# Performance work log

Measured on AMD Instinct MI355X. Metric: run time of the kernel, lower is better.

Reference implementation:

```python
import jax, jax.numpy as jnp
import numpy as np
from jax import lax

IN_CH = 512
OUT_CH = 512
HEAD_DIM = 8
NUM_HEADS = IN_CH // HEAD_DIM  # 64
INNER = NUM_HEADS * HEAD_DIM   # 512
KSIZE = 5
EPS = 1e-15
BN_EPS = 1e-5
DN = ('NCHW', 'OIHW', 'NCHW')


def setup_inputs() -> dict:
    key = jax.random.key(0)
    ks = jax.random.split(key, 10)
    s = 0.02
    return {
        'hidden_states': jax.random.normal(ks[0], (4, IN_CH, 64, 64), jnp.float32),
        'wq': jax.random.normal(ks[1], (INNER, IN_CH), jnp.float32) * s,
        'wk': jax.random.normal(ks[2], (INNER, IN_CH), jnp.float32) * s,
        'wv': jax.random.normal(ks[3], (INNER, IN_CH), jnp.float32) * s,
        # depthwise conv: groups = 3*INNER, 1 in-channel per group
        'dw_kernel': jax.random.normal(ks[4], (3 * INNER, 1, KSIZE, KSIZE), jnp.float32) * s,
        # grouped 1x1 conv: groups = 3*NUM_HEADS -> 3*INNER/(3*NUM_HEADS)=HEAD_DIM in-ch/group
        'pw_kernel': jax.random.normal(ks[5], (3 * INNER, HEAD_DIM, 1, 1), jnp.float32) * s,
        # proj_out 1x1: in = INNER*(1+len(kernel_sizes)) = 2*INNER
        'proj_kernel': jax.random.normal(ks[6], (OUT_CH, 2 * INNER, 1, 1), jnp.float32) * s,
        'bn_gamma': jnp.ones((OUT_CH,), jnp.float32),
        'bn_beta': jnp.zeros((OUT_CH,), jnp.float32),
        'bn_mean': jnp.zeros((OUT_CH,), jnp.float32),
        'bn_var': jnp.ones((OUT_CH,), jnp.float32),
    }


def _forward(hidden_states, wq, wk, wv, dw_kernel, pw_kernel, proj_kernel,
             bn_gamma, bn_beta, bn_mean, bn_var):
    x = hidden_states  # [B,C,H,W]
    B, _, H, W = x.shape
    h = jnp.moveaxis(x, 1, -1)  # [B,H,W,C]
    q = h @ wq.T
    k = h @ wk.T
    v = h @ wv.T
    qkv = jnp.moveaxis(jnp.concatenate([q, k, v], axis=-1), -1, 1)  # [B,3*INNER,H,W]

    # multi-scale aggregation: depthwise 5x5 then grouped 1x1
    dw = lax.conv_general_dilated(qkv, dw_kernel, (1, 1), 'SAME',
                                  feature_group_count=3 * INNER, dimension_numbers=DN)
    pw = lax.conv_general_dilated(dw, pw_kernel, (1, 1), 'VALID',
                                  feature_group_count=3 * NUM_HEADS, dimension_numbers=DN)
    qkv_all = jnp.concatenate([qkv, pw], axis=1)  # [B, 2*3*INNER, H, W]

    # relu linear attention (fp32)
    N = H * W
    d = HEAD_DIM
    f = qkv_all.astype(jnp.float32).reshape(B, -1, 3 * d, N)  # [B, nh_total, 3d, N]
    query = jax.nn.relu(f[:, :, :d])
    key_ = jax.nn.relu(f[:, :, d:2 * d])
    value = f[:, :, 2 * d:]
    value_pad = jnp.concatenate([value, jnp.ones_like(value[:, :, :1])], axis=2)  # [B,nh,d+1,N]
    scores = jnp.einsum('bhdn,bhen->bhde', value_pad, key_)   # [B,nh,d+1,d]
    out = jnp.einsum('bhde,bhen->bhdn', scores, query)         # [B,nh,d+1,N]
    out = out[:, :, :-1] / (out[:, :, -1:] + EPS)
    out = out.reshape(B, -1, H, W).astype(qkv_all.dtype)        # [B, 2*INNER, H, W]

    # proj_out 1x1 conv + BatchNorm2d (eval mode, running stats)
    y = lax.conv_general_dilated(out, proj_kernel, (1, 1), 'VALID', dimension_numbers=DN)
    inv = bn_gamma / jnp.sqrt(bn_var + BN_EPS)
    y = y * inv[None, :, None, None] + (bn_beta - bn_mean * inv)[None, :, None, None]
    return y + x


def reference(hidden_states, wq, wk, wv, dw_kernel, pw_kernel, proj_kernel,
              bn_gamma, bn_beta, bn_mean, bn_var):
    return _forward(hidden_states, wq, wk, wv, dw_kernel, pw_kernel, proj_kernel,
                    bn_gamma, bn_beta, bn_mean, bn_var)
```

## Files before the change

### kernel.cpp

```cpp
#include <hip/hip_runtime.h>
#include <hip/hip_bf16.h>

typedef __hip_bfloat16 bf16;
typedef __attribute__((ext_vector_type(8))) short bf16x8;
typedef __attribute__((ext_vector_type(4))) float f32x4;
typedef __attribute__((ext_vector_type(2))) float f32x2;

#define BATCH 4
#define CIN   512
#define HW    64
#define NPIX  4096
#define CALL  3072
#define NHEAD 128
#define EPS_LITE 1e-15f
#define BN_EPS   1e-5f
#define LDK   40


__device__ __forceinline__ short f2bf(float f) {
    __hip_bfloat16 h = __float2bfloat16(f);
    short s; __builtin_memcpy(&s, &h, 2); return s;
}
__device__ __forceinline__ float bfl(unsigned u) {
    unsigned v = u << 16; float f; __builtin_memcpy(&f, &v, 4); return f;
}
__device__ __forceinline__ float bfh(unsigned u) {
    unsigned v = u & 0xffff0000u; float f; __builtin_memcpy(&f, &v, 4); return f;
}
__device__ __forceinline__ unsigned packbf(float a, float b) {
    return (unsigned)(unsigned short)f2bf(a) | ((unsigned)(unsigned short)f2bf(b) << 16);
}

template<bool XF32, int KD, bool PROJ>
__global__ __launch_bounds__(256) void k_gemm(
        const void* __restrict__ Xv,
        const float* __restrict__ w0, const float* __restrict__ w1,
        const float* __restrict__ w2,
        bf16* __restrict__ Obf,
        const float* __restrict__ gm, const float* __restrict__ bt,
        const float* __restrict__ mu, const float* __restrict__ va,
        const float* __restrict__ resid, float* __restrict__ Of)
{
    constexpr int NT = KD / 32;
    __shared__ short Ald[2][64 * LDK];
    __shared__ short Bld[2][128 * LDK];

    const int t    = threadIdx.x;
    const int lane = t & 63;
    const int wid  = t >> 6;
    const int wm   = wid >> 1;
    const int wn   = wid & 1;
    const int n0   = blockIdx.x * 128;
    const int c0   = blockIdx.y * 64;
    const int b    = blockIdx.z;

    const float* W; int cr;
    if (PROJ)           { W = w0; cr = c0; }
    else if (c0 < 512)  { W = w0; cr = c0; }
    else if (c0 < 1024) { W = w1; cr = c0 - 512; }
    else                { W = w2; cr = c0 - 1024; }

    const int ca  = t >> 2;
    const int kga = t & 3;
    const int nb  = (t & 63) * 2;
    const int kgb = t >> 6;

    const float* aptr = W + (size_t)(cr + ca) * KD + kga * 8;
    const float* bpf  = (const float*)Xv + ((size_t)b * KD + kgb * 8) * NPIX + n0 + nb;
    const short* bph  = (const short*)Xv + ((size_t)b * KD + kgb * 8) * NPIX + n0 + nb;

    float areg[8];
    float br0[8], br1[8];
    unsigned bu[8];

    auto gload = [&]() {
        f32x4 a0 = *(const f32x4*)(aptr);
        f32x4 a1 = *(const f32x4*)(aptr + 4);
#pragma unroll
        for (int j = 0; j < 4; ++j) { areg[j] = a0[j]; areg[4 + j] = a1[j]; }
        if (XF32) {
#pragma unroll
            for (int j = 0; j < 8; ++j) {
                f32x2 v = *(const f32x2*)(bpf + (size_t)j * NPIX);
                br0[j] = v[0]; br1[j] = v[1];
            }
        } else {
#pragma unroll
            for (int j = 0; j < 8; ++j)
                bu[j] = *(const unsigned*)(bph + (size_t)j * NPIX);
        }
        aptr += 32;
        bpf += (size_t)32 * NPIX;
        bph += (size_t)32 * NPIX;
    };

    auto swrite = [&](int buf) {
        bf16x8 av, b0v, b1v;
#pragma unroll
        for (int j = 0; j < 8; ++j) av[j] = f2bf(areg[j]);
        if (XF32) {
#pragma unroll
            for (int j = 0; j < 8; ++j) { b0v[j] = f2bf(br0[j]); b1v[j] = f2bf(br1[j]); }
        } else {
#pragma unroll
            for (int j = 0; j < 8; ++j) {
                b0v[j] = (short)(bu[j] & 0xffff);
                b1v[j] = (short)(bu[j] >> 16);
            }
        }
        *(bf16x8*)&Ald[buf][ca * LDK + kga * 8]       = av;
        *(bf16x8*)&Bld[buf][nb * LDK + kgb * 8]       = b0v;
        *(bf16x8*)&Bld[buf][(nb + 1) * LDK + kgb * 8] = b1v;
    };

    f32x4 acc[2][4];
#pragma unroll
    for (int ms = 0; ms < 2; ++ms)
#pragma unroll
        for (int ns = 0; ns < 4; ++ns)
#pragma unroll
            for (int j = 0; j < 4; ++j) acc[ms][ns][j] = 0.f;

    gload();
    swrite(0);
    __syncthreads();

    const int l15 = lane & 15, l4 = lane >> 4;
    for (int s = 0; s < NT; ++s) {
        const int cur = s & 1;
        const bool pf = (s + 1 < NT);
        if (pf) gload();

        bf16x8 af[2], bfr[4];
#pragma unroll
        for (int ms = 0; ms < 2; ++ms)
            af[ms] = *(const bf16x8*)&Ald[cur][(wm * 32 + ms * 16 + l15) * LDK + l4 * 8];
#pragma unroll
        for (int ns = 0; ns < 4; ++ns)
            bfr[ns] = *(const bf16x8*)&Bld[cur][(wn * 64 + ns * 16 + l15) * LDK + l4 * 8];
#pragma unroll
        for (int ms = 0; ms < 2; ++ms)
#pragma unroll
            for (int ns = 0; ns < 4; ++ns)
                acc[ms][ns] = __builtin_amdgcn_mfma_f32_16x16x32_bf16(
                    af[ms], bfr[ns], acc[ms][ns], 0, 0, 0);

        if (pf) swrite(cur ^ 1);
        __syncthreads();
    }

    if (!PROJ) {
#pragma unroll
        for (int ms = 0; ms < 2; ++ms) {
            const int crow = c0 + wm * 32 + ms * 16 + l4 * 4;
#pragma unroll
            for (int ns = 0; ns < 4; ++ns) {
                const int ncol = n0 + wn * 64 + ns * 16 + l15;
#pragma unroll
                for (int j = 0; j < 4; ++j) {
                    bf16 h; short sv = f2bf(acc[ms][ns][j]);
                    __builtin_memcpy(&h, &sv, 2);
                    Obf[((size_t)b * CALL + crow + j) * NPIX + ncol] = h;
                }
            }
        }
    } else {
#pragma unroll
        for (int ms = 0; ms < 2; ++ms) {
            const int crow = c0 + wm * 32 + ms * 16 + l4 * 4;
#pragma unroll
            for (int j = 0; j < 4; ++j) {
                const int o = crow + j;
                const float inv = gm[o] / sqrtf(va[o] + BN_EPS);
                const float sh  = bt[o] - mu[o] * inv;
#pragma unroll
                for (int ns = 0; ns < 4; ++ns) {
                    const int ncol = n0 + wn * 64 + ns * 16 + l15;
                    const size_t idx = ((size_t)b * 512 + o) * NPIX + ncol;
                    Of[idx] = acc[ms][ns][j] * inv + sh + resid[idx];
                }
            }
        }
    }
}

__global__ __launch_bounds__(256) void k_dwpw(const float* __restrict__ dwk,
                                              const float* __restrict__ pwk,
                                              bf16* __restrict__ qkv_all) {
    __shared__ short in_lds[8 * 20 * 80];
    __shared__ short dw_lds[8 * 16 * 64];

    const int t  = threadIdx.x;
    const int g  = blockIdx.y;
    const int b  = blockIdx.z;
    const int y0 = blockIdx.x * 16;

    const bf16* src = qkv_all + ((size_t)b * CALL + g * 8) * NPIX;
#pragma unroll
    for (int i = 0; i < 7; ++i) {
        const int v = i * 256 + t;
        if (v < 1600) {
            const int ch  = v / 200;
            const int rem = v % 200;
            const int row = rem / 10;
            const int seg = rem % 10;
            const int grow = y0 + row - 2;
            uint4 val = make_uint4(0u, 0u, 0u, 0u);
            if (seg >= 1 && seg <= 8 && grow >= 0 && grow < HW)
                val = *(const uint4*)(src + (size_t)ch * NPIX + grow * HW + (seg - 1) * 8);
            *(uint4*)&in_lds[ch * 1600 + row * 80 + seg * 8] = val;
        }
    }

    const int lane = t & 63;
    const int w    = t >> 6;
    const int xb   = lane & 7;
    const int ch   = lane >> 3;
    const int x0   = xb * 8;

    float kc[25];
    {
        const float* kp = dwk + (size_t)(g * 8 + ch) * 25;
#pragma unroll
        for (int i = 0; i < 25; ++i) kc[i] = kp[i];
    }
    __syncthreads();

    float A[5][12];
    const short* cb = &in_lds[ch * 1600 + x0];

    auto loadrow = [&](int L, float* f) {
        const short* rp = cb + L * 80;
        uint2 lo = *(const uint2*)(rp + 4);
        uint4 md = *(const uint4*)(rp + 8);
        uint2 hi = *(const uint2*)(rp + 16);
        f[0]  = bfl(lo.y); f[1]  = bfh(lo.y);
        f[2]  = bfl(md.x); f[3]  = bfh(md.x);
        f[4]  = bfl(md.y); f[5]  = bfh(md.y);
        f[6]  = bfl(md.z); f[7]  = bfh(md.z);
        f[8]  = bfl(md.w); f[9]  = bfh(md.w);
        f[10] = bfl(hi.x); f[11] = bfh(hi.x);
    };

    const int r0 = w * 4;
    loadrow(r0 + 0, A[0]);
    loadrow(r0 + 1, A[1]);
    loadrow(r0 + 2, A[2]);
    loadrow(r0 + 3, A[3]);

#pragma unroll
    for (int ri = 0; ri < 4; ++ri) {
        loadrow(r0 + ri + 4, A[(ri + 4) % 5]);
        float acc[8];
#pragma unroll
        for (int i = 0; i < 8; ++i) acc[i] = 0.f;
#pragma unroll
        for (int dy = 0; dy < 5; ++dy) {
            const float* Ar = A[(ri + dy) % 5];
#pragma unroll
            for (int dx = 0; dx < 5; ++dx) {
                const float kv = kc[dy * 5 + dx];
#pragma unroll
                for (int i = 0; i < 8; ++i)
                    acc[i] += Ar[i + dx] * kv;
            }
        }
        uint4 pk;
        pk.x = packbf(acc[0], acc[1]);
        pk.y = packbf(acc[2], acc[3]);
        pk.z = packbf(acc[4], acc[5]);
        pk.w = packbf(acc[6], acc[7]);
        *(uint4*)&dw_lds[ch * 1024 + (r0 + ri) * 64 + x0] = pk;
    }
    __syncthreads();

    const float* pwb = pwk + (size_t)g * 64;
#pragma unroll
    for (int it = 0; it < 2; ++it) {
        const int p2 = (it * 256 + t) * 2;
        float v0[8], v1[8];
#pragma unroll
        for (int ci = 0; ci < 8; ++ci) {
            const unsigned u = *(const unsigned*)&dw_lds[ci * 1024 + p2];
            v0[ci] = bfl(u); v1[ci] = bfh(u);
        }
        bf16* op = qkv_all + ((size_t)b * CALL + 1536 + g * 8) * NPIX + y0 * HW + p2;
#pragma unroll
        for (int o = 0; o < 8; ++o) {
            float s0 = 0.f, s1 = 0.f;
#pragma unroll
            for (int ci = 0; ci < 8; ++ci) {
                const float wv = pwb[o * 8 + ci];
                s0 += wv * v0[ci]; s1 += wv * v1[ci];
            }
            *(unsigned*)(op + (size_t)o * NPIX) = packbf(s0, s1);
        }
    }
}

__global__ __launch_bounds__(64) void k_scores(const bf16* __restrict__ qkv_all,
                                               float* __restrict__ part) {
    const int lane = threadIdx.x;
    const int h = blockIdx.y;
    const int b = blockIdx.z;
    const bf16* base = qkv_all + ((size_t)b * CALL + h * 24) * NPIX;

    float acc[72];
#pragma unroll
    for (int i = 0; i < 72; ++i) acc[i] = 0.f;

    for (int it = 0; it < 4; ++it) {
        const int n = blockIdx.x * 512 + it * 128 + lane * 2;
        const bf16* p = base + n;
        float k0[8], k1[8], v0[8], v1[8];
#pragma unroll
        for (int e = 0; e < 8; ++e) {
            const unsigned u = *(const unsigned*)&p[(size_t)(8 + e) * NPIX];
            k0[e] = fmaxf(bfl(u), 0.f); k1[e] = fmaxf(bfh(u), 0.f);
        }
#pragma unroll
        for (int d = 0; d < 8; ++d) {
            const unsigned u = *(const unsigned*)&p[(size_t)(16 + d) * NPIX];
            v0[d] = bfl(u); v1[d] = bfh(u);
        }
#pragma unroll
        for (int d = 0; d < 9; ++d) {
            const float vd0 = (d < 8) ? v0[d] : 1.f;
            const float vd1 = (d < 8) ? v1[d] : 1.f;
#pragma unroll
            for (int e = 0; e < 8; ++e)
                acc[d * 8 + e] += vd0 * k0[e] + vd1 * k1[e];
        }
    }

    const int bh = b * NHEAD + h;
#pragma unroll
    for (int i = 0; i < 72; ++i) {
        float v = acc[i];
        for (int off = 32; off; off >>= 1) v += __shfl_xor(v, off, 64);
        if (lane == 0) part[((size_t)bh * 72 + i) * 8 + blockIdx.x] = v;
    }
}

__global__ __launch_bounds__(128) void k_scores2(const float* __restrict__ part,
                                                 float* __restrict__ scores) {
    const int bh = blockIdx.x;
    const int i = threadIdx.x;
    if (i < 72) {
        float s = 0.f;
#pragma unroll
        for (int ns = 0; ns < 8; ++ns) s += part[((size_t)bh * 72 + i) * 8 + ns];
        scores[(size_t)bh * 72 + i] = s;
    }
}

__global__ __launch_bounds__(256) void k_att(const bf16* __restrict__ qkv_all,
                                             const float* __restrict__ scores,
                                             bf16* __restrict__ att) {
    const int n2 = (blockIdx.x * 256 + threadIdx.x) * 2;
    const int h = blockIdx.y;
    const int b = blockIdx.z;

    const bf16* qb = qkv_all + ((size_t)b * CALL + h * 24) * NPIX + n2;
    float q0[8], q1[8];
#pragma unroll
    for (int e = 0; e < 8; ++e) {
        const unsigned u = *(const unsigned*)&qb[(size_t)e * NPIX];
        q0[e] = fmaxf(bfl(u), 0.f); q1[e] = fmaxf(bfh(u), 0.f);
    }

    const float* sp = scores + (size_t)(b * NHEAD + h) * 72;
    float n0[9], n1[9];
#pragma unroll
    for (int d = 0; d < 9; ++d) {
        float s0 = 0.f, s1 = 0.f;
#pragma unroll
        for (int e = 0; e < 8; ++e) {
            const float wv = sp[d * 8 + e];
            s0 += wv * q0[e]; s1 += wv * q1[e];
        }
        n0[d] = s0; n1[d] = s1;
    }
    const float i0 = 1.f / (n0[8] + EPS_LITE);
    const float i1 = 1.f / (n1[8] + EPS_LITE);
    bf16* op = att + ((size_t)b * 1024 + h * 8) * NPIX + n2;
#pragma unroll
    for (int d = 0; d < 8; ++d)
        *(unsigned*)(op + (size_t)d * NPIX) = packbf(n0[d] * i0, n1[d] * i1);
}

extern "C" void kernel_launch(void* const* d_in, const int* in_sizes, int n_in,
                              void* d_out, int out_size, void* d_ws, size_t ws_size,
                              hipStream_t stream) {
    const float* x   = (const float*)d_in[0];
    const float* wq  = (const float*)d_in[1];
    const float* wk  = (const float*)d_in[2];
    const float* wv  = (const float*)d_in[3];
    const float* dwk = (const float*)d_in[4];
    const float* pwk = (const float*)d_in[5];
    const float* pj  = (const float*)d_in[6];
    const float* gm  = (const float*)d_in[7];
    const float* bt  = (const float*)d_in[8];
    const float* mu  = (const float*)d_in[9];
    const float* va  = (const float*)d_in[10];
    float* out = (float*)d_out;

    char* ws = (char*)d_ws;
    bf16*  qkv_all = (bf16*)(ws);
    bf16*  att     = (bf16*)(ws + 100663296);
    float* part    = (float*)(ws + 134217728);
    float* scores  = (float*)(ws + 135397376);

    k_gemm<true, 512, false><<<dim3(32, 24, BATCH), 256, 0, stream>>>(
        x, wq, wk, wv, qkv_all, nullptr, nullptr, nullptr, nullptr, nullptr, nullptr);
    k_dwpw   <<<dim3( 4, 192, BATCH), 256, 0, stream>>>(dwk, pwk, qkv_all);
    k_scores <<<dim3( 8, 128, BATCH),  64, 0, stream>>>(qkv_all, part);
    k_scores2<<<dim3(512), 128, 0, stream>>>(part, scores);
    k_att    <<<dim3( 8, 128, BATCH), 256, 0, stream>>>(qkv_all, scores, att);
    k_gemm<false, 1024, true><<<dim3(32, 8, BATCH), 256, 0, stream>>>(
        att, pj, pj, pj, nullptr, gm, bt, mu, va, x, out);
}
```

Before: 191.8 us.

## Pre-convert weights to bf16 and widen GEMM tiles with direct-to-LDS loads

A small kernel now converts the QKV and projection weights to bf16 once per call. Both GEMMs then use a new kernel with 128x128 output tiles instead of 64x128, so each block reuses activation loads across twice as many output channels. The weight tiles are copied straight into LDS with global_load_lds, while the activation tile is staged through registers into a single-buffered LDS area. The cost is an extra launch, more accumulator registers per thread, half as many blocks, and a pipeline that depends on the compiler inserting the waits needed for the asynchronous LDS loads.

```diff
diff --git a/kernel.cpp b/kernel.cpp
--- a/kernel.cpp
+++ b/kernel.cpp
@@ -4,7 +4,6 @@
 typedef __hip_bfloat16 bf16;
 typedef __attribute__((ext_vector_type(8))) short bf16x8;
 typedef __attribute__((ext_vector_type(4))) float f32x4;
-typedef __attribute__((ext_vector_type(2))) float f32x2;
 
 #define BATCH 4
 #define CIN   512
@@ -14,7 +13,7 @@
 #define NHEAD 128
 #define EPS_LITE 1e-15f
 #define BN_EPS   1e-5f
-#define LDK   40
+#define LDKB  40
 
 
 __device__ __forceinline__ short f2bf(float f) {
@@ -31,128 +30,144 @@
     return (unsigned)(unsigned short)f2bf(a) | ((unsigned)(unsigned short)f2bf(b) << 16);
 }
 
+__device__ __forceinline__ void gll16(const void* gsrc, void* ldst) {
+    __builtin_amdgcn_global_load_lds(
+        (const __attribute__((address_space(1))) unsigned int*)gsrc,
+        (__attribute__((address_space(3))) unsigned int*)ldst, 16, 0, 0);
+}
+
+__global__ __launch_bounds__(256) void k_cvtw(const float* __restrict__ wq,
+                                              const float* __restrict__ wk,
+                                              const float* __restrict__ wv,
+                                              const float* __restrict__ pj,
+                                              bf16* __restrict__ Wbf,
+                                              bf16* __restrict__ Pbf) {
+    const int e = (blockIdx.x * 256 + threadIdx.x) * 4;
+    const float* s; bf16* dst;
+    if (e < 786432) {
+        int o;
+        if (e < 262144)      { s = wq; o = e; }
+        else if (e < 524288) { s = wk; o = e - 262144; }
+        else                 { s = wv; o = e - 524288; }
+        f32x4 v = *(const f32x4*)(s + o);
+        dst = Wbf + e;
+        ushort2 a = make_ushort2((unsigned short)f2bf(v[0]), (unsigned short)f2bf(v[1]));
+        ushort2 b = make_ushort2((unsigned short)f2bf(v[2]), (unsigned short)f2bf(v[3]));
+        *(ushort2*)dst = a; *(ushort2*)(dst + 2) = b;
+    } else {
+        const int o = e - 786432;
+        f32x4 v = *(const f32x4*)(pj + o);
+        dst = Pbf + o;
+        ushort2 a = make_ushort2((unsigned short)f2bf(v[0]), (unsigned short)f2bf(v[1]));
+        ushort2 b = make_ushort2((unsigned short)f2bf(v[2]), (unsigned short)f2bf(v[3]));
+        *(ushort2*)dst = a; *(ushort2*)(dst + 2) = b;
+    }
+}
+
 template<bool XF32, int KD, bool PROJ>
-__global__ __launch_bounds__(256) void k_gemm(
+__global__ __launch_bounds__(256) void k_gemm2(
         const void* __restrict__ Xv,
-        const float* __restrict__ w0, const float* __restrict__ w1,
-        const float* __restrict__ w2,
+        const bf16* __restrict__ Wb,
         bf16* __restrict__ Obf,
         const float* __restrict__ gm, const float* __restrict__ bt,
         const float* __restrict__ mu, const float* __restrict__ va,
         const float* __restrict__ resid, float* __restrict__ Of)
 {
     constexpr int NT = KD / 32;
-    __shared__ short Ald[2][64 * LDK];
-    __shared__ short Bld[2][128 * LDK];
+    __shared__ short Ald[2][128 * 32];
+    __shared__ short Bld[128 * LDKB];
 
     const int t    = threadIdx.x;
     const int lane = t & 63;
-    const int wid  = t >> 6;
-    const int wm   = wid >> 1;
-    const int wn   = wid & 1;
+    const int w    = t >> 6;
+    const int wm   = w >> 1;
+    const int wn   = w & 1;
     const int n0   = blockIdx.x * 128;
-    const int c0   = blockIdx.y * 64;
+    const int c0   = blockIdx.y * 128;
     const int b    = blockIdx.z;
 
-    const float* W; int cr;
-    if (PROJ)           { W = w0; cr = c0; }
-    else if (c0 < 512)  { W = w0; cr = c0; }
-    else if (c0 < 1024) { W = w1; cr = c0 - 512; }
-    else                { W = w2; cr = c0 - 1024; }
-
-    const int ca  = t >> 2;
-    const int kga = t & 3;
-    const int nb  = (t & 63) * 2;
-    const int kgb = t >> 6;
-
-    const float* aptr = W + (size_t)(cr + ca) * KD + kga * 8;
-    const float* bpf  = (const float*)Xv + ((size_t)b * KD + kgb * 8) * NPIX + n0 + nb;
-    const short* bph  = (const short*)Xv + ((size_t)b * KD + kgb * 8) * NPIX + n0 + nb;
-
-    float areg[8];
-    float br0[8], br1[8];
-    unsigned bu[8];
-
-    auto gload = [&]() {
-        f32x4 a0 = *(const f32x4*)(aptr);
-        f32x4 a1 = *(const f32x4*)(aptr + 4);
-#pragma unroll
-        for (int j = 0; j < 4; ++j) { areg[j] = a0[j]; areg[4 + j] = a1[j]; }
+    const int arow = lane >> 2;
+    const int akg  = lane & 3;
+    const bf16* abase = Wb + (size_t)(c0 + w * 32 + arow) * KD + akg * 8;
+
+    auto gllA = [&](int s, int buf) {
+#pragma unroll
+        for (int q = 0; q < 2; ++q)
+            gll16(abase + (size_t)q * 16 * KD + s * 32,
+                  &Ald[buf][(w * 32 + q * 16) * 32]);
+    };
+
+    const int brow = t & 127;
+    const int bkh  = t >> 7;
+    const float* bxf = (const float*)Xv + ((size_t)b * KD + bkh * 16) * NPIX + n0 + brow;
+    const unsigned short* bxh =
+        (const unsigned short*)Xv + ((size_t)b * KD + bkh * 16) * NPIX + n0 + brow;
+
+    float bregf[16]; unsigned short bregh[16];
+    auto bload = [&](int s) {
         if (XF32) {
 #pragma unroll
-            for (int j = 0; j < 8; ++j) {
-                f32x2 v = *(const f32x2*)(bpf + (size_t)j * NPIX);
-                br0[j] = v[0]; br1[j] = v[1];
-            }
+            for (int i = 0; i < 16; ++i) bregf[i] = bxf[((size_t)s * 32 + i) * NPIX];
         } else {
 #pragma unroll
-            for (int j = 0; j < 8; ++j)
-                bu[j] = *(const unsigned*)(bph + (size_t)j * NPIX);
-        }
-        aptr += 32;
-        bpf += (size_t)32 * NPIX;
-        bph += (size_t)32 * NPIX;
+            for (int i = 0; i < 16; ++i) bregh[i] = bxh[((size_t)s * 32 + i) * NPIX];
+        }
     };
-
-    auto swrite = [&](int buf) {
-        bf16x8 av, b0v, b1v;
-#pragma unroll
-        for (int j = 0; j < 8; ++j) av[j] = f2bf(areg[j]);
+    auto bwrite = [&]() {
+        bf16x8 p0, p1;
         if (XF32) {
 #pragma unroll
-            for (int j = 0; j < 8; ++j) { b0v[j] = f2bf(br0[j]); b1v[j] = f2bf(br1[j]); }
+            for (int j = 0; j < 8; ++j) { p0[j] = f2bf(bregf[j]); p1[j] = f2bf(bregf[8 + j]); }
         } else {
 #pragma unroll
-            for (int j = 0; j < 8; ++j) {
-                b0v[j] = (short)(bu[j] & 0xffff);
-                b1v[j] = (short)(bu[j] >> 16);
-            }
-        }
-        *(bf16x8*)&Ald[buf][ca * LDK + kga * 8]       = av;
-        *(bf16x8*)&Bld[buf][nb * LDK + kgb * 8]       = b0v;
-        *(bf16x8*)&Bld[buf][(nb + 1) * LDK + kgb * 8] = b1v;
+            for (int j = 0; j < 8; ++j) { p0[j] = (short)bregh[j]; p1[j] = (short)bregh[8 + j]; }
+        }
+        *(bf16x8*)&Bld[brow * LDKB + bkh * 16]     = p0;
+        *(bf16x8*)&Bld[brow * LDKB + bkh * 16 + 8] = p1;
     };
 
-    f32x4 acc[2][4];
-#pragma unroll
-    for (int ms = 0; ms < 2; ++ms)
+    f32x4 acc[4][4];
+#pragma unroll
+    for (int ms = 0; ms < 4; ++ms)
 #pragma unroll
         for (int ns = 0; ns < 4; ++ns)
 #pragma unroll
             for (int j = 0; j < 4; ++j) acc[ms][ns][j] = 0.f;
 
-    gload();
-    swrite(0);
-    __syncthreads();
+    gllA(0, 0);
+    bload(0);
 
     const int l15 = lane & 15, l4 = lane >> 4;
     for (int s = 0; s < NT; ++s) {
         const int cur = s & 1;
-        const bool pf = (s + 1 < NT);
-        if (pf) gload();
-
-        bf16x8 af[2], bfr[4];
-#pragma unroll
-        for (int ms = 0; ms < 2; ++ms)
-            af[ms] = *(const bf16x8*)&Ald[cur][(wm * 32 + ms * 16 + l15) * LDK + l4 * 8];
+        bwrite();
+        __syncthreads();
+        if (s + 1 < NT) {
+            gllA(s + 1, cur ^ 1);
+            bload(s + 1);
+        }
+
+        bf16x8 af[4], bv[4];
+#pragma unroll
+        for (int ms = 0; ms < 4; ++ms)
+            af[ms] = *(const bf16x8*)&Ald[cur][(wm * 64 + ms * 16 + l15) * 32 + l4 * 8];
 #pragma unroll
         for (int ns = 0; ns < 4; ++ns)
-            bfr[ns] = *(const bf16x8*)&Bld[cur][(wn * 64 + ns * 16 + l15) * LDK + l4 * 8];
-#pragma unroll
-        for (int ms = 0; ms < 2; ++ms)
+            bv[ns] = *(const bf16x8*)&Bld[(wn * 64 + ns * 16 + l15) * LDKB + l4 * 8];
+#pragma unroll
+        for (int ms = 0; ms < 4; ++ms)
 #pragma unroll
             for (int ns = 0; ns < 4; ++ns)
                 acc[ms][ns] = __builtin_amdgcn_mfma_f32_16x16x32_bf16(
-                    af[ms], bfr[ns], acc[ms][ns], 0, 0, 0);
-
-        if (pf) swrite(cur ^ 1);
+                    af[ms], bv[ns], acc[ms][ns], 0, 0, 0);
+
         __syncthreads();
     }
 
     if (!PROJ) {
 #pragma unroll
-        for (int ms = 0; ms < 2; ++ms) {
-            const int crow = c0 + wm * 32 + ms * 16 + l4 * 4;
+        for (int ms = 0; ms < 4; ++ms) {
+            const int crow = c0 + wm * 64 + ms * 16 + l4 * 4;
 #pragma unroll
             for (int ns = 0; ns < 4; ++ns) {
                 const int ncol = n0 + wn * 64 + ns * 16 + l15;
@@ -166,8 +181,8 @@
         }
     } else {
 #pragma unroll
-        for (int ms = 0; ms < 2; ++ms) {
-            const int crow = c0 + wm * 32 + ms * 16 + l4 * 4;
+        for (int ms = 0; ms < 4; ++ms) {
+            const int crow = c0 + wm * 64 + ms * 16 + l4 * 4;
 #pragma unroll
             for (int j = 0; j < 4; ++j) {
                 const int o = crow + j;
@@ -410,13 +425,16 @@
     bf16*  att     = (bf16*)(ws + 100663296);
     float* part    = (float*)(ws + 134217728);
     float* scores  = (float*)(ws + 135397376);
-
-    k_gemm<true, 512, false><<<dim3(32, 24, BATCH), 256, 0, stream>>>(
-        x, wq, wk, wv, qkv_all, nullptr, nullptr, nullptr, nullptr, nullptr, nullptr);
+    bf16*  Wbf     = (bf16*)(ws + 135544832);
+    bf16*  Pbf     = (bf16*)(ws + 137117696);
+
+    k_cvtw<<<dim3(1280), 256, 0, stream>>>(wq, wk, wv, pj, Wbf, Pbf);
+    k_gemm2<true, 512, false><<<dim3(32, 12, BATCH), 256, 0, stream>>>(
+        x, Wbf, qkv_all, nullptr, nullptr, nullptr, nullptr, nullptr, nullptr);
     k_dwpw   <<<dim3( 4, 192, BATCH), 256, 0, stream>>>(dwk, pwk, qkv_all);
     k_scores <<<dim3( 8, 128, BATCH),  64, 0, stream>>>(qkv_all, part);
     k_scores2<<<dim3(512), 128, 0, stream>>>(part, scores);
     k_att    <<<dim3( 8, 128, BATCH), 256, 0, stream>>>(qkv_all, scores, att);
-    k_gemm<false, 1024, true><<<dim3(32, 8, BATCH), 256, 0, stream>>>(
-        att, pj, pj, pj, nullptr, gm, bt, mu, va, x, out);
-}
+    k_gemm2<false, 1024, true><<<dim3(32, 4, BATCH), 256, 0, stream>>>(
+        att, Pbf, nullptr, gm, bt, mu, va, x, out);
+}
```

New measurement: 191.9 us. About the same (+0.0%).
